# Kernel optimization log

Hardware: AMD Instinct MI355X
Metric: run time of the kernel (lower is better)

The kernel has to match this reference:

```python
import jax, jax.numpy as jnp
import numpy as np


def setup_inputs() -> dict:
    key = jax.random.key(0)
    k_x, k_q, k_k, k_v = jax.random.split(key, 4)
    B, S, E, D = 4, 2048, 1024, 1024
    scale = 1.0 / np.sqrt(E)
    return {
        "x": jax.random.normal(k_x, (B, S, E), dtype=jnp.float32),
        # nn.Linear weight matrices, shape [out_dim, in_dim]; y = x @ W.T
        "w_q": jax.random.normal(k_q, (D, E), dtype=jnp.float32) * scale,
        "w_k": jax.random.normal(k_k, (D, E), dtype=jnp.float32) * scale,
        "w_v": jax.random.normal(k_v, (D, E), dtype=jnp.float32) * scale,
    }


def reference(x, w_q, w_k, w_v):
    # x: [B, S, E]; w_*: [D, E] (torch nn.Linear convention)
    B, S, E = x.shape
    q = jnp.einsum("bse,de->bsd", x, w_q)  # [B, S, D]
    k = jnp.einsum("bse,de->bsd", x, w_k)
    v = jnp.einsum("bse,de->bsd", x, w_v)
    D = q.shape[-1]
    # raw scores, then causal mask (strictly upper triangle -> -inf), then
    # scale by 1/sqrt(D) inside softmax exactly as the original does.
    scores = jnp.einsum("bsd,btd->bst", q, k)  # [B, S, S]
    causal = jnp.tril(jnp.ones((S, S), dtype=bool))  # True = keep
    scores = jnp.where(causal[None], scores, -jnp.inf)
    attn = jax.nn.softmax(scores / jnp.sqrt(jnp.asarray(D, x.dtype)), axis=-1)
    # dropout p=0.0 -> identity
    return jnp.einsum("bst,btd->bsd", attn, v)  # [B, S, D]
```

## Files before the change

### kernel.cpp

```cpp
#include <hip/hip_runtime.h>
#include <hip/hip_bf16.h>


typedef unsigned short u16;
typedef __attribute__((ext_vector_type(4))) u16   u16x4;
typedef __attribute__((ext_vector_type(8))) u16   u16x8;
typedef __attribute__((ext_vector_type(8))) short short8;
typedef __attribute__((ext_vector_type(4))) float f32x4;
typedef __attribute__((ext_vector_type(4))) int   i32x4;

__device__ inline u16 f2b(float v) {
    __hip_bfloat16 b = __float2bfloat16(v);
    return *reinterpret_cast<u16*>(&b);
}
__device__ inline float b2f(u16 v) {
    unsigned int u = ((unsigned int)v) << 16;
    return *reinterpret_cast<float*>(&u);
}

template <typename T> __device__ inline void store_elem(T* p, float v);
template <> __device__ inline void store_elem<float>(float* p, float v) { *p = v; }
template <> __device__ inline void store_elem<u16>(u16* p, float v)     { *p = f2b(v); }

__device__ inline void gload_lds16(const u16* g, u16* l) {
    __builtin_amdgcn_global_load_lds(
        (const __attribute__((address_space(1))) void*)g,
        (__attribute__((address_space(3))) void*)l, 16, 0, 0);
}

__global__ __launch_bounds__(256) void cast_all_kernel(
    const float* __restrict__ x,  const float* __restrict__ wq,
    const float* __restrict__ wk, const float* __restrict__ wv,
    u16* __restrict__ dst) {
    int q = blockIdx.x * 256 + threadIdx.x;
    const float* src;
    int sidx;
    if (q < 2097152) { src = x; sidx = q * 4; }
    else {
        int qq = q - 2097152;
        int w  = qq >> 18;
        sidx   = (qq & 262143) * 4;
        src    = (w == 0) ? wq : (w == 1) ? wk : wv;
    }
    float4 v = *(const float4*)(src + sidx);
    u16x4 o;
    o.x = f2b(v.x); o.y = f2b(v.y); o.z = f2b(v.z); o.w = f2b(v.w);
    *(u16x4*)(dst + q * 4) = o;
}

#define MT 128
#define NT 128
#define BKH 32
#define HSZ (MT * BKH)

template <int MODE, typename OutT>
__device__ __forceinline__ void gemm_bt_body(
    const u16* __restrict__ A, long long strideA, int lda,
    const u16* __restrict__ B, long long strideB, int ldb,
    OutT* __restrict__ C, long long strideC, int ldc,
    int M, int N, int K)
{
    int m0, n0;
    if (MODE == 1) {
        int t = blockIdx.x;
        float ff = sqrtf(8.0f * t + 1.0f);
        int m = (int)((ff - 1.0f) * 0.5f);
        while ((m + 1) * (m + 2) / 2 <= t) m++;
        while (m * (m + 1) / 2 > t) m--;
        m0 = m * MT;
        n0 = (t - m * (m + 1) / 2) * NT;
    } else if (MODE == 2) {
        m0 = (gridDim.y - 1 - blockIdx.y) * MT;
        n0 = blockIdx.x * NT;
    } else {
        m0 = blockIdx.y * MT;
        n0 = blockIdx.x * NT;
    }
    int Keff = K;
    if (MODE == 2) Keff = min(K, m0 + MT);

    const u16* Ab = A + (long long)blockIdx.z * strideA;
    const u16* Bb = B + (long long)blockIdx.z * strideB;
    OutT*      Cb = C + (long long)blockIdx.z * strideC;

    __shared__ __align__(16) u16 As[2 * HSZ];
    __shared__ __align__(16) u16 Bs[2 * HSZ];

    const int tid  = threadIdx.x;
    const int lane = tid & 63;
    const int wave = tid >> 6;
    const int quad = lane >> 4;
    const int r16  = lane & 15;
    const int mw   = (wave >> 1) * 64;
    const int nw   = (wave & 1) * 64;

    const int c0 = tid, c1 = tid + 256;
    const int r0 = c0 >> 2, k0 = (c0 & 3) * 8;
    const int r1 = c1 >> 2, k1 = (c1 & 3) * 8;
    const u16* a0 = Ab + (long long)(m0 + r0) * lda + k0;
    const u16* a1 = Ab + (long long)(m0 + r1) * lda + k1;
    const u16* b0 = Bb + (long long)(n0 + r0) * ldb + k0;
    const u16* b1 = Bb + (long long)(n0 + r1) * ldb + k1;

    f32x4 acc[4][4] = {};

    for (int kk = 0; kk < Keff; kk += 2 * BKH) {
        __syncthreads();
        gload_lds16(a0 + kk,        &As[c0 * 8]);
        gload_lds16(a1 + kk,        &As[c1 * 8]);
        gload_lds16(a0 + kk + BKH,  &As[HSZ + c0 * 8]);
        gload_lds16(a1 + kk + BKH,  &As[HSZ + c1 * 8]);
        gload_lds16(b0 + kk,        &Bs[c0 * 8]);
        gload_lds16(b1 + kk,        &Bs[c1 * 8]);
        gload_lds16(b0 + kk + BKH,  &Bs[HSZ + c0 * 8]);
        gload_lds16(b1 + kk + BKH,  &Bs[HSZ + c1 * 8]);
        __syncthreads();

#pragma unroll
        for (int h = 0; h < 2; h++) {
            short8 af[4], bf[4];
#pragma unroll
            for (int i = 0; i < 4; i++)
                af[i] = *(const short8*)&As[h * HSZ + (mw + i * 16 + r16) * BKH + quad * 8];
#pragma unroll
            for (int j = 0; j < 4; j++)
                bf[j] = *(const short8*)&Bs[h * HSZ + (nw + j * 16 + r16) * BKH + quad * 8];
#pragma unroll
            for (int i = 0; i < 4; i++)
#pragma unroll
                for (int j = 0; j < 4; j++)
                    acc[i][j] = __builtin_amdgcn_mfma_f32_16x16x32_bf16(af[i], bf[j], acc[i][j], 0, 0, 0);
        }
    }

#pragma unroll
    for (int i = 0; i < 4; i++)
#pragma unroll
        for (int j = 0; j < 4; j++)
#pragma unroll
            for (int r = 0; r < 4; r++) {
                int m = m0 + mw + i * 16 + quad * 4 + r;
                int n = n0 + nw + j * 16 + r16;
                store_elem(&Cb[(long long)m * ldc + n], acc[i][j][r]);
            }
}

__global__ __launch_bounds__(256) void gemm_qkv(
    const u16* A, long long sA, int lda, const u16* B, long long sB, int ldb,
    u16* C, long long sC, int ldc, int M, int N, int K) {
    gemm_bt_body<0, u16>(A, sA, lda, B, sB, ldb, C, sC, ldc, M, N, K);
}
__global__ __launch_bounds__(256) void gemm_scores(
    const u16* A, long long sA, int lda, const u16* B, long long sB, int ldb,
    u16* C, long long sC, int ldc, int M, int N, int K) {
    gemm_bt_body<1, u16>(A, sA, lda, B, sB, ldb, C, sC, ldc, M, N, K);
}
__global__ __launch_bounds__(256) void gemm_pv(
    const u16* A, long long sA, int lda, const u16* B, long long sB, int ldb,
    float* C, long long sC, int ldc, int M, int N, int K) {
    gemm_bt_body<2, float>(A, sA, lda, B, sB, ldb, C, sC, ldc, M, N, K);
}

__global__ __launch_bounds__(256) void softmax_kernel(const u16* __restrict__ sc,
                                                      u16* __restrict__ P) {
    const int S = 2048;
    int row = blockIdx.x;
    int i   = row & (S - 1);
    int n   = i + 1;
    const u16* srow = sc + (long long)row * S;
    u16*       prow = P  + (long long)row * S;

    int j0 = threadIdx.x * 8;
    u16x8 raw = *(const u16x8*)(srow + j0);
    float v[8];
#pragma unroll
    for (int e = 0; e < 8; e++) v[e] = (j0 + e < n) ? b2f(raw[e]) : -1e30f;

    __shared__ float red[8];
    float lmax = v[0];
#pragma unroll
    for (int e = 1; e < 8; e++) lmax = fmaxf(lmax, v[e]);
    for (int o = 32; o > 0; o >>= 1) lmax = fmaxf(lmax, __shfl_xor(lmax, o, 64));
    int wid = threadIdx.x >> 6;
    if ((threadIdx.x & 63) == 0) red[wid] = lmax;
    __syncthreads();
    float Mx = fmaxf(fmaxf(red[0], red[1]), fmaxf(red[2], red[3]));

    const float C = 0.045112384f;
    float ev[8];
    float lsum = 0.f;
#pragma unroll
    for (int e = 0; e < 8; e++) {
        ev[e] = (j0 + e < n) ? exp2f((v[e] - Mx) * C) : 0.f;
        lsum += ev[e];
    }
    for (int o = 32; o > 0; o >>= 1) lsum += __shfl_xor(lsum, o, 64);
    if ((threadIdx.x & 63) == 0) red[4 + wid] = lsum;
    __syncthreads();
    float inv = 1.0f / (red[4] + red[5] + red[6] + red[7]);

    u16x8 o8;
#pragma unroll
    for (int e = 0; e < 8; e++) o8[e] = f2b(ev[e] * inv);
    *(u16x8*)(prow + j0) = o8;
}

__global__ __launch_bounds__(256) void transpose_v_kernel(const u16* __restrict__ qkv,
                                                          u16* __restrict__ vt) {
    int b  = blockIdx.z;
    int s0 = blockIdx.x * 64;
    int d0 = blockIdx.y * 64;
    __shared__ __align__(16) u16 tile[64][80];
    int tid = threadIdx.x;
    for (int c = tid; c < 512; c += 256) {
        int r = c >> 3, c8 = (c & 7) * 8;
        *(i32x4*)&tile[r][c8] =
            *(const i32x4*)(qkv + (long long)(b * 2048 + s0 + r) * 3072 + 2048 + d0 + c8);
    }
    __syncthreads();
    for (int c = tid; c < 512; c += 256) {
        int dd = c >> 3, s8 = (c & 7) * 8;
        alignas(16) u16 tmp[8];
#pragma unroll
        for (int e = 0; e < 8; e++) tmp[e] = tile[s8 + e][dd];
        *(i32x4*)(vt + ((long long)b * 1024 + d0 + dd) * 2048 + s0 + s8) = *(i32x4*)tmp;
    }
}

extern "C" void kernel_launch(void* const* d_in, const int* in_sizes, int n_in,
                              void* d_out, int out_size, void* d_ws, size_t ws_size,
                              hipStream_t stream) {
    const float* x  = (const float*)d_in[0];
    const float* wq = (const float*)d_in[1];
    const float* wk = (const float*)d_in[2];
    const float* wv = (const float*)d_in[3];
    float* out = (float*)d_out;

    char* ws = (char*)d_ws;
    u16* xb  = (u16*)(ws);
    u16* wb  = (u16*)(ws + 16777216LL);
    u16* qkv = (u16*)(ws + 23068672LL);
    u16* sc  = (u16*)(ws + 73400320LL);
    u16* P   = (u16*)(ws + 106954752LL);
    u16* vt  = (u16*)(ws + 140509184LL);

    cast_all_kernel<<<11264, 256, 0, stream>>>(x, wq, wk, wv, xb);

    gemm_qkv<<<dim3(24, 64, 1), 256, 0, stream>>>(
        xb, 0, 1024, wb, 0, 1024, qkv, 0, 3072, 8192, 3072, 1024);

    transpose_v_kernel<<<dim3(32, 16, 4), 256, 0, stream>>>(qkv, vt);

    gemm_scores<<<dim3(136, 1, 4), 256, 0, stream>>>(
        qkv,        2048LL * 3072, 3072,
        qkv + 1024, 2048LL * 3072, 3072,
        sc,         2048LL * 2048, 2048, 2048, 2048, 1024);

    softmax_kernel<<<8192, 256, 0, stream>>>(sc, P);

    gemm_pv<<<dim3(8, 16, 4), 256, 0, stream>>>(
        P,  2048LL * 2048, 2048,
        vt, 1024LL * 2048, 2048,
        out, 2048LL * 1024, 1024, 2048, 1024, 2048);
}
```

Before: 267.6 us.

## Split causal PV GEMM along K for load balance and combine partials

Replaces the triangular-K PV GEMM with a split-K scheme. Row tiles in the lower half of the sequence split their K range into two 1024-wide chunks. Blocks are ordered longest-first so the 192x4 grid is more evenly loaded than the original 128x4 grid, where late row tiles carried up to 16x the work. Partial results for the second chunk go to a workspace buffer and are added in by a separate combine kernel, which costs an extra launch and extra fp32 traffic.

```diff
diff --git a/kernel.cpp b/kernel.cpp
--- a/kernel.cpp
+++ b/kernel.cpp
@@ -69,15 +69,10 @@
         while (m * (m + 1) / 2 > t) m--;
         m0 = m * MT;
         n0 = (t - m * (m + 1) / 2) * NT;
-    } else if (MODE == 2) {
-        m0 = (gridDim.y - 1 - blockIdx.y) * MT;
-        n0 = blockIdx.x * NT;
     } else {
         m0 = blockIdx.y * MT;
         n0 = blockIdx.x * NT;
     }
-    int Keff = K;
-    if (MODE == 2) Keff = min(K, m0 + MT);
 
     const u16* Ab = A + (long long)blockIdx.z * strideA;
     const u16* Bb = B + (long long)blockIdx.z * strideB;
@@ -104,7 +99,7 @@
 
     f32x4 acc[4][4] = {};
 
-    for (int kk = 0; kk < Keff; kk += 2 * BKH) {
+    for (int kk = 0; kk < K; kk += 2 * BKH) {
         __syncthreads();
         gload_lds16(a0 + kk,        &As[c0 * 8]);
         gload_lds16(a1 + kk,        &As[c1 * 8]);
@@ -155,10 +150,106 @@
     u16* C, long long sC, int ldc, int M, int N, int K) {
     gemm_bt_body<1, u16>(A, sA, lda, B, sB, ldb, C, sC, ldc, M, N, K);
 }
+
 __global__ __launch_bounds__(256) void gemm_pv(
-    const u16* A, long long sA, int lda, const u16* B, long long sB, int ldb,
-    float* C, long long sC, int ldc, int M, int N, int K) {
-    gemm_bt_body<2, float>(A, sA, lda, B, sB, ldb, C, sC, ldc, M, N, K);
+    const u16* __restrict__ P, const u16* __restrict__ vt,
+    float* __restrict__ out, float* __restrict__ part)
+{
+    const int bid = blockIdx.x;
+    int m, chunk, n;
+    if (bid < 80) {
+        int q = bid >> 3; n = bid & 7;
+        if (q < 9) { m = 7 + q; chunk = 0; } else { m = 15; chunk = 1; }
+    } else {
+        int r = bid - 80; int s = 7 - (r >> 4); int t = r & 15;
+        n = t & 7;
+        if (t < 8) { m = s - 1; chunk = 0; } else { m = s + 7; chunk = 1; }
+    }
+    const int m0 = m * MT, n0 = n * NT;
+    const int kbeg = chunk ? 1024 : 0;
+    const int kend = chunk ? (m0 + MT) : min(1024, m0 + MT);
+    const int b = blockIdx.z;
+
+    const u16* Ab = P  + (long long)b * 2048 * 2048;
+    const u16* Bb = vt + (long long)b * 1024 * 2048;
+
+    __shared__ __align__(16) u16 As[2 * HSZ];
+    __shared__ __align__(16) u16 Bs[2 * HSZ];
+
+    const int tid  = threadIdx.x;
+    const int lane = tid & 63;
+    const int wave = tid >> 6;
+    const int quad = lane >> 4;
+    const int r16  = lane & 15;
+    const int mw   = (wave >> 1) * 64;
+    const int nw   = (wave & 1) * 64;
+
+    const int c0 = tid, c1 = tid + 256;
+    const int r0 = c0 >> 2, k0 = (c0 & 3) * 8;
+    const int r1 = c1 >> 2, k1 = (c1 & 3) * 8;
+    const u16* a0 = Ab + (long long)(m0 + r0) * 2048 + k0;
+    const u16* a1 = Ab + (long long)(m0 + r1) * 2048 + k1;
+    const u16* b0 = Bb + (long long)(n0 + r0) * 2048 + k0;
+    const u16* b1 = Bb + (long long)(n0 + r1) * 2048 + k1;
+
+    f32x4 acc[4][4] = {};
+
+    for (int kk = kbeg; kk < kend; kk += 2 * BKH) {
+        __syncthreads();
+        gload_lds16(a0 + kk,        &As[c0 * 8]);
+        gload_lds16(a1 + kk,        &As[c1 * 8]);
+        gload_lds16(a0 + kk + BKH,  &As[HSZ + c0 * 8]);
+        gload_lds16(a1 + kk + BKH,  &As[HSZ + c1 * 8]);
+        gload_lds16(b0 + kk,        &Bs[c0 * 8]);
+        gload_lds16(b1 + kk,        &Bs[c1 * 8]);
+        gload_lds16(b0 + kk + BKH,  &Bs[HSZ + c0 * 8]);
+        gload_lds16(b1 + kk + BKH,  &Bs[HSZ + c1 * 8]);
+        __syncthreads();
+
+#pragma unroll
+        for (int h = 0; h < 2; h++) {
+            short8 af[4], bf[4];
+#pragma unroll
+            for (int i = 0; i < 4; i++)
+                af[i] = *(const short8*)&As[h * HSZ + (mw + i * 16 + r16) * BKH + quad * 8];
+#pragma unroll
+            for (int j = 0; j < 4; j++)
+                bf[j] = *(const short8*)&Bs[h * HSZ + (nw + j * 16 + r16) * BKH + quad * 8];
+#pragma unroll
+            for (int i = 0; i < 4; i++)
+#pragma unroll
+                for (int j = 0; j < 4; j++)
+                    acc[i][j] = __builtin_amdgcn_mfma_f32_16x16x32_bf16(af[i], bf[j], acc[i][j], 0, 0, 0);
+        }
+    }
+
+#pragma unroll
+    for (int i = 0; i < 4; i++)
+#pragma unroll
+        for (int j = 0; j < 4; j++)
+#pragma unroll
+            for (int r = 0; r < 4; r++) {
+                int mg = m0 + mw + i * 16 + quad * 4 + r;
+                int ng = n0 + nw + j * 16 + r16;
+                if (chunk == 0)
+                    out[(long long)b * 2097152 + (long long)mg * 1024 + ng] = acc[i][j][r];
+                else
+                    part[(long long)b * 1048576 + (long long)(mg - 1024) * 1024 + ng] = acc[i][j][r];
+            }
+}
+
+__global__ __launch_bounds__(256) void pv_combine(float* __restrict__ out,
+                                                  const float* __restrict__ part) {
+    long long idx = ((long long)blockIdx.x * 256 + threadIdx.x) * 8;
+    long long bb = idx >> 20;
+    long long j  = idx & 1048575;
+    float* o = out + bb * 2097152 + 1048576 + j;
+    const float* p = part + bb * 1048576 + j;
+    float4 o0 = *(float4*)o, o1 = *(float4*)(o + 4);
+    float4 p0 = *(const float4*)p, p1 = *(const float4*)(p + 4);
+    o0.x += p0.x; o0.y += p0.y; o0.z += p0.z; o0.w += p0.w;
+    o1.x += p1.x; o1.y += p1.y; o1.z += p1.z; o1.w += p1.w;
+    *(float4*)o = o0; *(float4*)(o + 4) = o1;
 }
 
 __global__ __launch_bounds__(256) void softmax_kernel(const u16* __restrict__ sc,
@@ -237,12 +328,13 @@
     float* out = (float*)d_out;
 
     char* ws = (char*)d_ws;
-    u16* xb  = (u16*)(ws);
-    u16* wb  = (u16*)(ws + 16777216LL);
-    u16* qkv = (u16*)(ws + 23068672LL);
-    u16* sc  = (u16*)(ws + 73400320LL);
-    u16* P   = (u16*)(ws + 106954752LL);
-    u16* vt  = (u16*)(ws + 140509184LL);
+    u16*   xb   = (u16*)(ws);
+    u16*   wb   = (u16*)(ws + 16777216LL);
+    u16*   qkv  = (u16*)(ws + 23068672LL);
+    u16*   sc   = (u16*)(ws + 73400320LL);
+    u16*   P    = (u16*)(ws + 106954752LL);
+    u16*   vt   = (u16*)(ws + 140509184LL);
+    float* part = (float*)(ws + 157286400LL);
 
     cast_all_kernel<<<11264, 256, 0, stream>>>(x, wq, wk, wv, xb);
 
@@ -258,8 +350,6 @@
 
     softmax_kernel<<<8192, 256, 0, stream>>>(sc, P);
 
-    gemm_pv<<<dim3(8, 16, 4), 256, 0, stream>>>(
-        P,  2048LL * 2048, 2048,
-        vt, 1024LL * 2048, 2048,
-        out, 2048LL * 1024, 1024, 2048, 1024, 2048);
-}
+    gemm_pv<<<dim3(192, 1, 4), 256, 0, stream>>>(P, vt, out, part);
+    pv_combine<<<2048, 256, 0, stream>>>(out, part);
+}
```

After: 266.7 us. No clear change (-0.3%).
